# Optimization experiments

Hardware: AMD Instinct MI355X
Metric: run time of the kernel (lower is better)

Reference implementation:

```python
import jax, jax.numpy as jnp
import numpy as np

N_HEAD = 16
D_LATENT = 64
N_EMBD = 1024
D_HEAD = N_EMBD // N_HEAD          # 64
D_HEAD_E = D_HEAD // 2             # 32 (rotary part)
D_HEAD_C = D_HEAD // 2             # 32 (content part)
BLOCK_SIZE = 1024


def rope_cache(dim, max_seq_len, theta=10000.0):
    inv_freq = 1.0 / (theta ** (jnp.arange(0, dim, 2, dtype=jnp.float32) / dim))
    t = jnp.arange(max_seq_len, dtype=jnp.float32)
    freqs = t[:, None] * inv_freq[None, :]            # [T, dim/2]
    emb = jnp.concatenate([freqs, freqs], axis=-1)    # [T, dim]
    return jnp.cos(emb), jnp.sin(emb)


def apply_rope(x, cos, sin):
    # x: [B, H, T, C]; interleaved rotate-half as in the torch module
    B, H, T, C = x.shape
    xf = x.astype(jnp.float32)
    xr = xf.reshape(B, H, T, C // 2, 2)
    x1, x2 = xr[..., 0], xr[..., 1]
    rotated = jnp.stack([-x2, x1], axis=-1).reshape(B, H, T, C)
    c = cos[:T][None, None]  # [1,1,T,C]
    s = sin[:T][None, None]
    return (xf * c + rotated * s).astype(x.dtype)


def setup_inputs() -> dict:
    key = jax.random.key(0)
    ks = jax.random.split(key, 10)
    std = 0.02
    inp = {
        "x": jax.random.normal(ks[0], (4, 1024, N_EMBD), dtype=jnp.float32),
        "Wq_down": jax.random.normal(ks[1], (N_EMBD, N_HEAD * D_LATENT), dtype=jnp.float32) * std,
        "Wk_down": jax.random.normal(ks[2], (N_EMBD, N_HEAD * D_LATENT), dtype=jnp.float32) * std,
        "Wv_down": jax.random.normal(ks[3], (N_EMBD, N_HEAD * D_LATENT), dtype=jnp.float32) * std,
        "Wq_up_c": jax.random.normal(ks[4], (D_LATENT, D_HEAD_C), dtype=jnp.float32) * std,
        "Wq_up_e": jax.random.normal(ks[5], (D_LATENT, D_HEAD_E), dtype=jnp.float32) * std,
        "Wk_up_c": jax.random.normal(ks[6], (D_LATENT, D_HEAD_C), dtype=jnp.float32) * std,
        "Wk_up_e": jax.random.normal(ks[7], (D_LATENT, D_HEAD_E), dtype=jnp.float32) * std,
        "Wv_up": jax.random.normal(ks[8], (D_LATENT, D_HEAD), dtype=jnp.float32) * std,
        "Wc": jax.random.normal(ks[9], (N_EMBD, N_EMBD), dtype=jnp.float32) * std,
    }
    return inp


def reference(x, Wq_down, Wk_down, Wv_down, Wq_up_c, Wq_up_e, Wk_up_c, Wk_up_e, Wv_up, Wc):
    B, T, C = x.shape
    # MLA down projections -> per-head latents [B, T, H, d_latent]
    q_lat = jnp.einsum('btc,cd->btd', x, Wq_down).reshape(B, T, N_HEAD, D_LATENT)
    k_lat = jnp.einsum('btc,cd->btd', x, Wk_down).reshape(B, T, N_HEAD, D_LATENT)
    v_lat = jnp.einsum('btc,cd->btd', x, Wv_down).reshape(B, T, N_HEAD, D_LATENT)
    # Up projections, fused with the transpose(1,2): [B, H, T, d]
    q_c = jnp.einsum('bthl,ld->bhtd', q_lat, Wq_up_c)
    q_e = jnp.einsum('bthl,ld->bhtd', q_lat, Wq_up_e)
    k_c = jnp.einsum('bthl,ld->bhtd', k_lat, Wk_up_c)
    k_e = jnp.einsum('bthl,ld->bhtd', k_lat, Wk_up_e)
    v = jnp.einsum('bthl,ld->bhtd', v_lat, Wv_up)
    # Partial RoPE on the 'e' halves
    cos, sin = rope_cache(D_HEAD_E, BLOCK_SIZE)
    q = jnp.concatenate([q_c, apply_rope(q_e, cos, sin)], axis=-1)  # [B,H,T,d_head]
    k = jnp.concatenate([k_c, apply_rope(k_e, cos, sin)], axis=-1)
    # Causal scaled dot-product attention (== SDPA is_causal=True, no dropout)
    scale = 1.0 / jnp.sqrt(jnp.array(q.shape[-1], dtype=jnp.float32))
    att = jnp.einsum('bhqd,bhkd->bhqk', q, k) * scale
    causal = jnp.tril(jnp.ones((T, T), dtype=bool))
    att = jnp.where(causal[None, None], att, jnp.float32(-1e30))
    att = jax.nn.softmax(att, axis=-1)
    y = jnp.einsum('bhqk,bhkd->bhqd', att, v)
    y = y.transpose(0, 2, 1, 3).reshape(B, T, C)
    y = jnp.einsum('btc,cd->btd', y, Wc)
    return y, k_lat, v_lat
```

## Files before the change

### kernel.cpp

```cpp
#include <hip/hip_runtime.h>

typedef unsigned short u16;
typedef unsigned int   u32;
typedef __bf16 bf16x8 __attribute__((ext_vector_type(8)));
typedef float  f32x4  __attribute__((ext_vector_type(4)));


__device__ __forceinline__ float b2f(u16 u) {
    u32 x = ((u32)u) << 16; float f; __builtin_memcpy(&f, &x, 4); return f;
}
__device__ __forceinline__ u16 f2b(float f) {
    u32 x; __builtin_memcpy(&x, &f, 4);
    u32 r = x + 0x7FFFu + ((x >> 16) & 1u);
    return (u16)(r >> 16);
}

#define GLD_LDS16(src, dst) \
  __builtin_amdgcn_global_load_lds((const __attribute__((address_space(1))) unsigned int*)(src), \
                                   (__attribute__((address_space(3))) unsigned int*)(dst), 16, 0, 0)

__global__ __launch_bounds__(256) void prep(
    const float* __restrict__ x, u16* __restrict__ xb,
    const float* __restrict__ W0, const float* __restrict__ W1,
    const float* __restrict__ W2, const float* __restrict__ W3,
    u16* __restrict__ T0, u16* __restrict__ T1,
    u16* __restrict__ T2, u16* __restrict__ T3)
{
    const int bx = blockIdx.x, tid = threadIdx.x;
    if (bx >= 1024) {
        int i0 = ((bx - 1024) * 256 + tid) * 8;
        #pragma unroll
        for (int j = 0; j < 8; j++) xb[i0 + j] = f2b(x[i0 + j]);
        return;
    }
    __shared__ u16 t[64][65];
    int z = bx >> 8, xy = bx & 255;
    const float* W = (z == 0) ? W0 : (z == 1) ? W1 : (z == 2) ? W2 : W3;
    u16* O = (z == 0) ? T0 : (z == 1) ? T1 : (z == 2) ? T2 : T3;
    int r0 = (xy >> 4) * 64, c0 = (xy & 15) * 64;
    int row = tid >> 2, seg = (tid & 3) * 16;
    #pragma unroll
    for (int i = 0; i < 16; i++)
        t[row][seg + i] = f2b(W[(size_t)(r0 + row) * 1024 + c0 + seg + i]);
    __syncthreads();
    #pragma unroll
    for (int i = 0; i < 16; i++)
        O[(size_t)(c0 + row) * 1024 + r0 + seg + i] = t[seg + i][row];
}

#define M97_GEMM_LOOP(A_, Bt_)                                                 \
    const int skb = (((l & 7) * 16) ^ ((l >> 3) << 4)) >> 1;                   \
    const int srow = l >> 3;                                                   \
    f32x4 acc[4][4] = {};                                                      \
    for (int kt = 0; kt < 16; ++kt) {                                          \
        const int k0 = kt * 64;                                                \
        if (kt > 0) __syncthreads();                                           \
        _Pragma("unroll")                                                      \
        for (int ci = 0; ci < 4; ++ci) {                                       \
            int c = w + ci * 4;                                                \
            int row = c * 8 + srow;                                            \
            GLD_LDS16(A_  + (size_t)(m0 + row) * K + k0 + skb, sA + c * 1024); \
            GLD_LDS16(Bt_ + (size_t)(n0 + row) * K + k0 + skb, sB + c * 1024); \
        }                                                                      \
        asm volatile("s_waitcnt vmcnt(0)" ::: "memory");                       \
        __syncthreads();                                                       \
        _Pragma("unroll")                                                      \
        for (int kk = 0; kk < 2; ++kk) {                                       \
            bf16x8 af[4], bf[4];                                               \
            _Pragma("unroll")                                                  \
            for (int mi = 0; mi < 4; ++mi) {                                   \
                int row = wr * 64 + mi * 16 + fr;                              \
                int off = row * 128 + ((kk * 64 + fg * 16) ^ ((fr & 7) << 4)); \
                af[mi] = *(const bf16x8*)(sA + off);                           \
            }                                                                  \
            _Pragma("unroll")                                                  \
            for (int ni = 0; ni < 4; ++ni) {                                   \
                int row = wc * 64 + ni * 16 + fr;                              \
                int off = row * 128 + ((kk * 64 + fg * 16) ^ ((fr & 7) << 4)); \
                bf[ni] = *(const bf16x8*)(sB + off);                           \
            }                                                                  \
            _Pragma("unroll")                                                  \
            for (int mi = 0; mi < 4; ++mi)                                     \
                _Pragma("unroll")                                              \
                for (int ni = 0; ni < 4; ++ni)                                 \
                    acc[mi][ni] = __builtin_amdgcn_mfma_f32_16x16x32_bf16(     \
                        af[mi], bf[ni], acc[mi][ni], 0, 0, 0);                 \
        }                                                                      \
    }

__global__ __launch_bounds__(256) void gemm_fused(
    const u16* __restrict__ A,
    const u16* __restrict__ Bt0, const u16* __restrict__ Bt1, const u16* __restrict__ Bt2,
    const float* __restrict__ Wqc, const float* __restrict__ Wqe,
    const float* __restrict__ Wkc, const float* __restrict__ Wke,
    const float* __restrict__ Wv,
    float* __restrict__ klat_out, float* __restrict__ vlat_out,
    u16* __restrict__ Qo, u16* __restrict__ Ko, u16* __restrict__ Vto)
{
    constexpr int K = 1024, N = 1024;
    __shared__ __align__(16) char smem[40960];
    char* sA = smem;
    char* sB = smem + 16384;
    u16 (*sW)[64][8] = (u16(*)[64][8])(smem + 32768);
    const int tid = threadIdx.x;
    const int w = tid >> 6, l = tid & 63;
    const int z = blockIdx.z;
    const u16* Bt = (z == 0) ? Bt0 : (z == 1) ? Bt1 : Bt2;
    const int m0 = blockIdx.x * 128, n0 = blockIdx.y * 128;
    const int wr = w >> 1, wc = w & 1;
    const int fr = l & 15, fg = l >> 4;

    for (int e = tid; e < 4096; e += 256) {
        int k = e >> 6, n = e & 63;
        float v;
        if (z == 2)      v = Wv[k * 64 + n];
        else if (z == 0) v = (n < 32) ? Wqc[k * 32 + n] : Wqe[k * 32 + n - 32];
        else             v = (n < 32) ? Wkc[k * 32 + n] : Wke[k * 32 + n - 32];
        sW[k >> 3][n][k & 7] = f2b(v);
    }

    M97_GEMM_LOOP(A, Bt)

    if (z) {
        float* L = (z == 1) ? klat_out : vlat_out;
        #pragma unroll
        for (int mi = 0; mi < 4; ++mi)
            #pragma unroll
            for (int ni = 0; ni < 4; ++ni)
                #pragma unroll
                for (int rr = 0; rr < 4; ++rr) {
                    int r = m0 + wr * 64 + mi * 16 + fg * 4 + rr;
                    int c = n0 + wc * 64 + ni * 16 + fr;
                    L[(size_t)r * N + c] = acc[mi][ni][rr];
                }
    }

    __syncthreads();

    char* sL = smem + w * 8192;
    #pragma unroll
    for (int mi = 0; mi < 4; ++mi)
        #pragma unroll
        for (int ni = 0; ni < 4; ++ni)
            #pragma unroll
            for (int rr = 0; rr < 4; ++rr) {
                int row = mi * 16 + fg * 4 + rr;
                int lat = ni * 16 + fr;
                int byte = row * 128 + ((((lat >> 3) ^ (row & 7)) << 4) | ((lat & 7) << 1));
                *(u16*)(sL + byte) = f2b(acc[mi][ni][rr]);
            }
    __syncthreads();

    bf16x8 af2[4][2], bf2[4][2];
    #pragma unroll
    for (int mi = 0; mi < 4; ++mi)
        #pragma unroll
        for (int kk = 0; kk < 2; ++kk) {
            int row = mi * 16 + fr;
            af2[mi][kk] = *(const bf16x8*)(sL + row * 128 + (((kk * 4 + fg) ^ (row & 7)) << 4));
        }
    #pragma unroll
    for (int ni = 0; ni < 4; ++ni)
        #pragma unroll
        for (int kk = 0; kk < 2; ++kk)
            bf2[ni][kk] = *(const bf16x8*)&sW[kk * 4 + fg][ni * 16 + fr][0];

    f32x4 o2[4][4] = {};
    #pragma unroll
    for (int kk = 0; kk < 2; ++kk)
        #pragma unroll
        for (int mi = 0; mi < 4; ++mi)
            #pragma unroll
            for (int ni = 0; ni < 4; ++ni)
                o2[mi][ni] = __builtin_amdgcn_mfma_f32_16x16x32_bf16(af2[mi][kk], bf2[ni][kk], o2[mi][ni], 0, 0, 0);

    const int rbase = m0 + wr * 64;
    const int b = rbase >> 10, tbase = rbase & 1023;
    const int h = blockIdx.y * 2 + wc;
    const size_t obase = ((size_t)(b * 16 + h)) << 16;

    if (z == 2) {
        #pragma unroll
        for (int mi = 0; mi < 4; ++mi)
            #pragma unroll
            for (int ni = 0; ni < 4; ++ni) {
                union { u16 u[4]; uint2 v; } pk;
                #pragma unroll
                for (int rr = 0; rr < 4; ++rr) pk.u[rr] = f2b(o2[mi][ni][rr]);
                int t0 = tbase + mi * 16 + fg * 4;
                int d = ni * 16 + fr;
                *(uint2*)(Vto + obase + (size_t)d * 1024 + t0) = pk.v;
            }
    } else {
        const float qscale = (z == 0) ? 0.125f : 1.0f;
        const float rf = __expf(-(float)fr * 0.5756462732485115f);
        u16* O = (z == 0) ? Qo : Ko;
        #pragma unroll
        for (int mi = 0; mi < 4; ++mi) {
            #pragma unroll
            for (int rr = 0; rr < 4; ++rr) {
                int t = tbase + mi * 16 + fg * 4 + rr;
                float ang = (float)t * rf;
                float sn = __sinf(ang), cs = __cosf(ang);
                #pragma unroll
                for (int ni = 0; ni < 4; ++ni) {
                    float a = o2[mi][ni][rr];
                    float p = __shfl_xor(a, 1);
                    if (ni >= 2)
                        a = a * cs + ((fr & 1) ? p : -p) * sn;
                    a *= qscale;
                    O[obase + (size_t)t * 64 + ni * 16 + fr] = f2b(a);
                }
            }
        }
    }
}

__global__ __launch_bounds__(256) void gemm128_out(
    const u16* __restrict__ A, const u16* __restrict__ Bt, float* __restrict__ Cf)
{
    constexpr int K = 1024, N = 1024;
    __shared__ __align__(16) char sA[16384];
    __shared__ __align__(16) char sB[16384];
    const int tid = threadIdx.x;
    const int w = tid >> 6, l = tid & 63;
    const int m0 = blockIdx.x * 128, n0 = blockIdx.y * 128;
    const int wr = w >> 1, wc = w & 1;
    const int fr = l & 15, fg = l >> 4;

    M97_GEMM_LOOP(A, Bt)

    #pragma unroll
    for (int mi = 0; mi < 4; ++mi)
        #pragma unroll
        for (int ni = 0; ni < 4; ++ni)
            #pragma unroll
            for (int rr = 0; rr < 4; ++rr) {
                int r = m0 + wr * 64 + mi * 16 + fg * 4 + rr;
                int c = n0 + wc * 64 + ni * 16 + fr;
                Cf[(size_t)r * N + c] = acc[mi][ni][rr];
            }
}

__global__ __launch_bounds__(256) void attn(
    const u16* __restrict__ Q, const u16* __restrict__ K,
    const u16* __restrict__ Vt, u16* __restrict__ Y)
{
    __shared__ __align__(16) char sK[2][8192];
    __shared__ __align__(16) char sV[2][8192];
    __shared__ __align__(16) char sP[4][2048];
    const int tid = threadIdx.x, w = tid >> 6, l = tid & 63;
    const int bh = blockIdx.x;
    const int qt = 15 - blockIdx.y;
    const int fr = l & 15, fg = l >> 4;
    const size_t base = (size_t)bh << 16;
    const int b = bh >> 4, h = bh & 15;
    const int q0w = qt * 64 + w * 16;

    const int skb = (((l & 7) * 16) ^ ((l >> 3) << 4)) >> 1;
    const int srow = l >> 3;

    bf16x8 qf[2];
    #pragma unroll
    for (int kk = 0; kk < 2; kk++)
        qf[kk] = *(const bf16x8*)(Q + base + (size_t)(q0w + fr) * 64 + kk * 32 + fg * 8);

    f32x4 o[4] = {};
    float m[4], ls[4] = {0.f, 0.f, 0.f, 0.f};
    #pragma unroll
    for (int rr = 0; rr < 4; rr++) m[rr] = -30000.0f;

    auto stage = [&](int buf, int kv0) {
        #pragma unroll
        for (int ci = 0; ci < 2; ++ci) {
            int c = w + ci * 4;
            int row = c * 8 + srow;
            GLD_LDS16(K  + base + (size_t)(kv0 + row) * 64 + skb, sK[buf] + c * 1024);
            GLD_LDS16(Vt + base + (size_t)row * 1024 + kv0 + skb, sV[buf] + c * 1024);
        }
    };

    stage(0, 0);
    asm volatile("s_waitcnt vmcnt(0)" ::: "memory");
    __syncthreads();
    int cur = 0;
    for (int kt = 0; kt <= qt; ++kt) {
        const int kv0 = kt * 64;
        if (kt < qt) stage(cur ^ 1, kv0 + 64);

        f32x4 s[4] = {};
        #pragma unroll
        for (int kk = 0; kk < 2; kk++)
            #pragma unroll
            for (int ni = 0; ni < 4; ni++) {
                int off = (ni * 16 + fr) * 128 + ((kk * 64 + fg * 16) ^ ((fr & 7) << 4));
                bf16x8 kf = *(const bf16x8*)(sK[cur] + off);
                s[ni] = __builtin_amdgcn_mfma_f32_16x16x32_bf16(qf[kk], kf, s[ni], 0, 0, 0);
            }
        if (kt == qt) {
            #pragma unroll
            for (int ni = 0; ni < 4; ni++) {
                int kj = kv0 + ni * 16 + fr;
                #pragma unroll
                for (int rr = 0; rr < 4; rr++) {
                    int qi = q0w + fg * 4 + rr;
                    if (kj > qi) s[ni][rr] = -30000.0f;
                }
            }
        }
        float alpha[4];
        #pragma unroll
        for (int rr = 0; rr < 4; rr++) {
            float mx = fmaxf(fmaxf(s[0][rr], s[1][rr]), fmaxf(s[2][rr], s[3][rr]));
            mx = fmaxf(mx, __shfl_xor(mx, 1));
            mx = fmaxf(mx, __shfl_xor(mx, 2));
            mx = fmaxf(mx, __shfl_xor(mx, 4));
            mx = fmaxf(mx, __shfl_xor(mx, 8));
            float mn = fmaxf(m[rr], mx);
            alpha[rr] = __expf(m[rr] - mn);
            m[rr] = mn;
        }
        float psum[4] = {0.f, 0.f, 0.f, 0.f};
        #pragma unroll
        for (int ni = 0; ni < 4; ni++)
            #pragma unroll
            for (int rr = 0; rr < 4; rr++) {
                float pv = __expf(s[ni][rr] - m[rr]);
                s[ni][rr] = pv;
                psum[rr] += pv;
            }
        #pragma unroll
        for (int rr = 0; rr < 4; rr++) ls[rr] = ls[rr] * alpha[rr] + psum[rr];
        #pragma unroll
        for (int ni = 0; ni < 4; ni++)
            #pragma unroll
            for (int rr = 0; rr < 4; rr++) o[ni][rr] *= alpha[rr];
        #pragma unroll
        for (int ni = 0; ni < 4; ni++)
            #pragma unroll
            for (int rr = 0; rr < 4; rr++) {
                int prow = fg * 4 + rr, col = ni * 16 + fr;
                *(u16*)(sP[w] + prow * 128 + ((col * 2) ^ ((prow & 7) << 4))) = f2b(s[ni][rr]);
            }
        #pragma unroll
        for (int kk = 0; kk < 2; kk++) {
            int poff = fr * 128 + ((kk * 64 + fg * 16) ^ ((fr & 7) << 4));
            bf16x8 pa = *(const bf16x8*)(sP[w] + poff);
            #pragma unroll
            for (int ni = 0; ni < 4; ni++) {
                int voff = (ni * 16 + fr) * 128 + ((kk * 64 + fg * 16) ^ ((fr & 7) << 4));
                bf16x8 vf = *(const bf16x8*)(sV[cur] + voff);
                o[ni] = __builtin_amdgcn_mfma_f32_16x16x32_bf16(pa, vf, o[ni], 0, 0, 0);
            }
        }
        asm volatile("s_waitcnt vmcnt(0)" ::: "memory");
        __syncthreads();
        cur ^= 1;
    }

    #pragma unroll
    for (int rr = 0; rr < 4; rr++) {
        float tot = ls[rr];
        tot += __shfl_xor(tot, 1);
        tot += __shfl_xor(tot, 2);
        tot += __shfl_xor(tot, 4);
        tot += __shfl_xor(tot, 8);
        ls[rr] = 1.0f / tot;
    }
    #pragma unroll
    for (int ni = 0; ni < 4; ni++)
        #pragma unroll
        for (int rr = 0; rr < 4; rr++) {
            int qi = q0w + fg * 4 + rr;
            size_t yoff = ((size_t)(b * 1024 + qi)) * 1024 + h * 64 + ni * 16 + fr;
            Y[yoff] = f2b(o[ni][rr] * ls[rr]);
        }
}

extern "C" void kernel_launch(void* const* d_in, const int* in_sizes, int n_in,
                              void* d_out, int out_size, void* d_ws, size_t ws_size,
                              hipStream_t stream) {
    const float* x    = (const float*)d_in[0];
    const float* Wqd  = (const float*)d_in[1];
    const float* Wkd  = (const float*)d_in[2];
    const float* Wvd  = (const float*)d_in[3];
    const float* Wqc  = (const float*)d_in[4];
    const float* Wqe  = (const float*)d_in[5];
    const float* Wkc  = (const float*)d_in[6];
    const float* Wke  = (const float*)d_in[7];
    const float* Wvu  = (const float*)d_in[8];
    const float* Wc   = (const float*)d_in[9];

    float* dout     = (float*)d_out;
    float* y_out    = dout;
    float* klat_out = dout + 4194304;
    float* vlat_out = dout + 8388608;

    const size_t MiB = 1024 * 1024;
    char* ws = (char*)d_ws;
    u16* WqdT = (u16*)(ws);
    u16* WkdT = (u16*)(ws + 2  * MiB);
    u16* WvdT = (u16*)(ws + 4  * MiB);
    u16* WcT  = (u16*)(ws + 6  * MiB);
    u16* xb   = (u16*)(ws + 8  * MiB);
    u16* Qw   = (u16*)(ws + 16 * MiB);
    u16* Kw   = (u16*)(ws + 24 * MiB);
    u16* Vtw  = (u16*)(ws + 32 * MiB);
    u16* Ya   = (u16*)(ws + 40 * MiB);

    prep<<<dim3(3072), 256, 0, stream>>>(x, xb, Wqd, Wkd, Wvd, Wc,
                                         WqdT, WkdT, WvdT, WcT);
    gemm_fused<<<dim3(32, 8, 3), 256, 0, stream>>>(xb, WqdT, WkdT, WvdT,
                                                   Wqc, Wqe, Wkc, Wke, Wvu,
                                                   klat_out, vlat_out,
                                                   Qw, Kw, Vtw);
    attn<<<dim3(64, 16), 256, 0, stream>>>(Qw, Kw, Vtw, Ya);
    gemm128_out<<<dim3(32, 8), 256, 0, stream>>>(Ya, WcT, y_out);
}
```

Before: 98.33 us.

## Load K and V fragments directly from global memory in attention

Removes the double-buffered LDS staging of K and V tiles and the per-iteration block-wide barrier. Each wave now loads its MFMA K and V fragments straight from global memory (relying on L1/L2) into registers. This cuts LDS usage and synchronization, but every wave now redundantly fetches the same K/V data and global latency is no longer overlapped with compute by explicit prefetch.

```diff
diff --git a/kernel.cpp b/kernel.cpp
--- a/kernel.cpp
+++ b/kernel.cpp
@@ -246,8 +246,6 @@
     const u16* __restrict__ Q, const u16* __restrict__ K,
     const u16* __restrict__ Vt, u16* __restrict__ Y)
 {
-    __shared__ __align__(16) char sK[2][8192];
-    __shared__ __align__(16) char sV[2][8192];
     __shared__ __align__(16) char sP[4][2048];
     const int tid = threadIdx.x, w = tid >> 6, l = tid & 63;
     const int bh = blockIdx.x;
@@ -257,9 +255,6 @@
     const int b = bh >> 4, h = bh & 15;
     const int q0w = qt * 64 + w * 16;
 
-    const int skb = (((l & 7) * 16) ^ ((l >> 3) << 4)) >> 1;
-    const int srow = l >> 3;
-
     bf16x8 qf[2];
     #pragma unroll
     for (int kk = 0; kk < 2; kk++)
@@ -270,33 +265,25 @@
     #pragma unroll
     for (int rr = 0; rr < 4; rr++) m[rr] = -30000.0f;
 
-    auto stage = [&](int buf, int kv0) {
-        #pragma unroll
-        for (int ci = 0; ci < 2; ++ci) {
-            int c = w + ci * 4;
-            int row = c * 8 + srow;
-            GLD_LDS16(K  + base + (size_t)(kv0 + row) * 64 + skb, sK[buf] + c * 1024);
-            GLD_LDS16(Vt + base + (size_t)row * 1024 + kv0 + skb, sV[buf] + c * 1024);
-        }
-    };
-
-    stage(0, 0);
-    asm volatile("s_waitcnt vmcnt(0)" ::: "memory");
-    __syncthreads();
-    int cur = 0;
+    const u16* Kb = K  + base + (size_t)fr * 64 + fg * 8;
+    const u16* Vb = Vt + base + (size_t)fr * 1024 + fg * 8;
+
     for (int kt = 0; kt <= qt; ++kt) {
         const int kv0 = kt * 64;
-        if (kt < qt) stage(cur ^ 1, kv0 + 64);
-
+
+        bf16x8 kf[2][4];
+        #pragma unroll
+        for (int kk = 0; kk < 2; kk++)
+            #pragma unroll
+            for (int ni = 0; ni < 4; ni++)
+                kf[kk][ni] = *(const bf16x8*)(Kb + (size_t)(kv0 + ni * 16) * 64 + kk * 32);
         f32x4 s[4] = {};
         #pragma unroll
         for (int kk = 0; kk < 2; kk++)
             #pragma unroll
-            for (int ni = 0; ni < 4; ni++) {
-                int off = (ni * 16 + fr) * 128 + ((kk * 64 + fg * 16) ^ ((fr & 7) << 4));
-                bf16x8 kf = *(const bf16x8*)(sK[cur] + off);
-                s[ni] = __builtin_amdgcn_mfma_f32_16x16x32_bf16(qf[kk], kf, s[ni], 0, 0, 0);
-            }
+            for (int ni = 0; ni < 4; ni++)
+                s[ni] = __builtin_amdgcn_mfma_f32_16x16x32_bf16(qf[kk], kf[kk][ni], s[ni], 0, 0, 0);
+
         if (kt == qt) {
             #pragma unroll
             for (int ni = 0; ni < 4; ni++) {
@@ -335,6 +322,7 @@
         for (int ni = 0; ni < 4; ni++)
             #pragma unroll
             for (int rr = 0; rr < 4; rr++) o[ni][rr] *= alpha[rr];
+
         #pragma unroll
         for (int ni = 0; ni < 4; ni++)
             #pragma unroll
@@ -342,20 +330,21 @@
                 int prow = fg * 4 + rr, col = ni * 16 + fr;
                 *(u16*)(sP[w] + prow * 128 + ((col * 2) ^ ((prow & 7) << 4))) = f2b(s[ni][rr]);
             }
+
+        bf16x8 vf[2][4];
+        #pragma unroll
+        for (int kk = 0; kk < 2; kk++)
+            #pragma unroll
+            for (int ni = 0; ni < 4; ni++)
+                vf[kk][ni] = *(const bf16x8*)(Vb + (size_t)(ni * 16) * 1024 + kv0 + kk * 32);
         #pragma unroll
         for (int kk = 0; kk < 2; kk++) {
             int poff = fr * 128 + ((kk * 64 + fg * 16) ^ ((fr & 7) << 4));
             bf16x8 pa = *(const bf16x8*)(sP[w] + poff);
             #pragma unroll
-            for (int ni = 0; ni < 4; ni++) {
-                int voff = (ni * 16 + fr) * 128 + ((kk * 64 + fg * 16) ^ ((fr & 7) << 4));
-                bf16x8 vf = *(const bf16x8*)(sV[cur] + voff);
-                o[ni] = __builtin_amdgcn_mfma_f32_16x16x32_bf16(pa, vf, o[ni], 0, 0, 0);
-            }
-        }
-        asm volatile("s_waitcnt vmcnt(0)" ::: "memory");
-        __syncthreads();
-        cur ^= 1;
+            for (int ni = 0; ni < 4; ni++)
+                o[ni] = __builtin_amdgcn_mfma_f32_16x16x32_bf16(pa, vf[kk][ni], o[ni], 0, 0, 0);
+        }
     }
 
     #pragma unroll
```

After: 136.3 us. +38.6%, slower.
